# Kernel optimization log

Measured on AMD Instinct MI355X. Metric: run time of the kernel, lower is better.

Reference implementation:

```python
import jax, jax.numpy as jnp
import numpy as np

EMBED_DIM = 1024
FFN_DIM = 4096
N_QUBITS = 10


def setup_inputs() -> dict:
    key = jax.random.key(0)
    k_x, k_phi, k_w1, k_w2 = jax.random.split(key, 4)
    x = jax.random.normal(k_x, (8, 2048, EMBED_DIM), dtype=jnp.float32)
    # trainable RY angles, one per wire (torchquantum init ~ U(0, 2pi); any init works for a reference)
    ry_params = jax.random.uniform(k_phi, (N_QUBITS,), dtype=jnp.float32, minval=0.0, maxval=2.0 * np.pi)
    # nn.Linear(n_qubits, ffn_dim, bias=False): weight [ffn_dim, n_qubits]
    w1 = jax.random.normal(k_w1, (FFN_DIM, N_QUBITS), dtype=jnp.float32) / np.sqrt(N_QUBITS)
    # nn.Linear(ffn_dim, embed_dim, bias=False): weight [embed_dim, ffn_dim]
    w2 = jax.random.normal(k_w2, (EMBED_DIM, FFN_DIM), dtype=jnp.float32) / np.sqrt(FFN_DIM)
    return {"x": x, "ry_params": ry_params, "w1": w1, "w2": w2}


def reference(x, ry_params, w1, w2):
    # Quantum layer in closed form: wires are unentangled.
    # |0> --RX(x_i)--RY(phi_i)--> <Z_i> = cos(x_i) * cos(phi_i)
    # Only the first N_QUBITS features of each token are encoded.
    q_out = jnp.cos(x[..., :N_QUBITS]) * jnp.cos(ry_params)  # [B, S, nq]
    # dropout is identity in eval mode
    h = jnp.einsum('bsq,fq->bsf', q_out, w1)  # [B, S, ffn]
    h = jax.nn.relu(h)
    return jnp.einsum('bsf,ef->bse', h, w2)  # [B, S, embed]
```

## Files before the change

### kernel.cpp

```cpp
#include <hip/hip_runtime.h>
#include <stdint.h>

#define M_TOK   16384
#define EMBED   1024
#define FFN     4096
#define NQ      10

#define GK 4096
#define GN 1024
#define BK 64
#define NT (GK / BK)

typedef __attribute__((ext_vector_type(8))) short  bf16x8;
typedef __attribute__((ext_vector_type(4))) float  f32x4;
typedef __attribute__((ext_vector_type(8))) unsigned short u16x8;

static __device__ __forceinline__ unsigned short f2bf(float f) {
    union { float f; unsigned u; } v; v.f = f;
    unsigned r = v.u + 0x7FFF + ((v.u >> 16) & 1);
    return (unsigned short)(r >> 16);
}

__global__ __launch_bounds__(256) void compute_h(
    const float* __restrict__ x, const float* __restrict__ ry,
    const float* __restrict__ w1, unsigned short* __restrict__ h)
{
    __shared__ float cq[32 * 16];
    __shared__ float cry[NQ];

    const int tid = threadIdx.x;
    const int t0  = blockIdx.x * 32;
    const int fb  = blockIdx.y * 2048 + tid * 8;

    if (tid < NQ) cry[tid] = cosf(ry[tid]);
    for (int idx = tid; idx < 32 * NQ; idx += 256) {
        int t = idx / NQ;
        int i = idx - t * NQ;
        cq[t * 16 + i] = cosf(x[(size_t)(t0 + t) * EMBED + i]);
    }
    __syncthreads();

    float wf[8][NQ];
#pragma unroll
    for (int fi = 0; fi < 8; ++fi)
#pragma unroll
        for (int i = 0; i < NQ; ++i)
            wf[fi][i] = w1[(fb + fi) * NQ + i] * cry[i];

    for (int t = 0; t < 32; ++t) {
        const float4 c0 = *(const float4*)&cq[t * 16 + 0];
        const float4 c1 = *(const float4*)&cq[t * 16 + 4];
        const float2 c2 = *(const float2*)&cq[t * 16 + 8];
        u16x8 v;
#pragma unroll
        for (int fi = 0; fi < 8; ++fi) {
            float s = c0.x * wf[fi][0] + c0.y * wf[fi][1] + c0.z * wf[fi][2]
                    + c0.w * wf[fi][3] + c1.x * wf[fi][4] + c1.y * wf[fi][5]
                    + c1.z * wf[fi][6] + c1.w * wf[fi][7] + c2.x * wf[fi][8]
                    + c2.y * wf[fi][9];
            v[fi] = f2bf(fmaxf(s, 0.f));
        }
        *(u16x8*)(h + (size_t)(t0 + t) * FFN + fb) = v;
    }
}

__global__ __launch_bounds__(256) void conv_w2(
    const float* __restrict__ w2, unsigned short* __restrict__ o)
{
    const int idx = (blockIdx.x * 256 + threadIdx.x) * 8;
    float4 a = *(const float4*)(w2 + idx);
    float4 b = *(const float4*)(w2 + idx + 4);
    u16x8 v;
    v[0] = f2bf(a.x); v[1] = f2bf(a.y); v[2] = f2bf(a.z); v[3] = f2bf(a.w);
    v[4] = f2bf(b.x); v[5] = f2bf(b.y); v[6] = f2bf(b.z); v[7] = f2bf(b.w);
    *(u16x8*)(o + idx) = v;
}

#define GL2LDS(g, l) \
    __builtin_amdgcn_global_load_lds( \
        (const __attribute__((address_space(1))) void*)(g), \
        (__attribute__((address_space(3))) void*)(l), 16, 0, 0)

__global__ __launch_bounds__(512, 2) void gemm_bt(
    const unsigned short* __restrict__ A,
    const unsigned short* __restrict__ B,
    float* __restrict__ C)
{
    __shared__ __align__(16) unsigned short As[2][256 * BK];
    __shared__ __align__(16) unsigned short Bs[2][256 * BK];

    const int tid  = threadIdx.x;
    const int wv   = tid >> 6;
    const int lane = tid & 63;
    const int wm   = wv >> 2;
    const int wn   = wv & 3;

    const int bid = blockIdx.x;
    const int wg  = (bid & 7) * 32 + (bid >> 3);
    const int m0  = (wg >> 2) * 256;
    const int n0  = (wg & 3) * 256;

    const int srow8 = lane >> 3;
    const int schk  = (lane & 7) ^ srow8;
    const char* ag = (const char*)A +
        ((size_t)(m0 + wv * 16 + srow8) * GK + schk * 8) * 2;
    const char* bg = (const char*)B +
        ((size_t)(n0 + wv * 16 + srow8) * GK + schk * 8) * 2;
    const size_t ROW8 = (size_t)8 * GK * 2;
    const size_t HALF = (size_t)128 * GK * 2;

#define STAGE_A(buf, half, ko) do { \
    GL2LDS(ag + (ko) + (half) * HALF,        (char*)As[buf] + ((half) * 128 + wv * 16) * 128); \
    GL2LDS(ag + (ko) + (half) * HALF + ROW8, (char*)As[buf] + ((half) * 128 + wv * 16 + 8) * 128); \
} while (0)
#define STAGE_B(buf, half, ko) do { \
    GL2LDS(bg + (ko) + (half) * HALF,        (char*)Bs[buf] + ((half) * 128 + wv * 16) * 128); \
    GL2LDS(bg + (ko) + (half) * HALF + ROW8, (char*)Bs[buf] + ((half) * 128 + wv * 16 + 8) * 128); \
} while (0)

    const int rr  = lane & 15;
    const int fsw = lane & 7;
    const int cc  = lane >> 4;
#define CHOFF(s) ((((s) * 4 + cc) ^ fsw) * 16)
#define AFRAG(mh, i, s) (*(const bf16x8*)(At + (wm * 128 + (mh) * 64 + (i) * 16 + rr) * 128 + CHOFF(s)))
#define BFRAG(nh, j, s) (*(const bf16x8*)(Bt + (wn * 64 + (nh) * 32 + (j) * 16 + rr) * 128 + CHOFF(s)))

    f32x4 acc[8][4] = {};

    STAGE_A(0, 0, 0); STAGE_A(0, 1, 0);
    STAGE_B(0, 0, 0); STAGE_B(0, 1, 0);
    asm volatile("s_waitcnt vmcnt(0)" ::: "memory");
    __builtin_amdgcn_s_barrier();

#pragma unroll 1
    for (int T = 0; T < NT; ++T) {
        const char* At = (const char*)As[T & 1];
        const char* Bt = (const char*)Bs[T & 1];
        const int nb   = (T + 1) & 1;
        const size_t ko = (size_t)(T + 1) * 128;
        const bool st  = (T + 1 < NT);

        bf16x8 afr[2][4];
        bf16x8 b0r[2][2];
        bf16x8 b1r[2][2];

#pragma unroll
        for (int s = 0; s < 2; ++s) {
#pragma unroll
            for (int i = 0; i < 4; ++i) afr[s][i] = AFRAG(0, i, s);
#pragma unroll
            for (int j = 0; j < 2; ++j) b0r[s][j] = BFRAG(0, j, s);
        }
        if (st) { STAGE_A(nb, 0, ko); STAGE_A(nb, 1, ko); }
        __builtin_amdgcn_s_barrier();
        asm volatile("s_waitcnt lgkmcnt(0)" ::: "memory");
        __builtin_amdgcn_sched_barrier(0);
        __builtin_amdgcn_s_setprio(1);
#pragma unroll
        for (int s = 0; s < 2; ++s)
#pragma unroll
            for (int i = 0; i < 4; ++i)
#pragma unroll
                for (int j = 0; j < 2; ++j)
                    acc[i][j] = __builtin_amdgcn_mfma_f32_16x16x32_bf16(
                        afr[s][i], b0r[s][j], acc[i][j], 0, 0, 0);
        __builtin_amdgcn_s_setprio(0);
        __builtin_amdgcn_s_barrier();

#pragma unroll
        for (int s = 0; s < 2; ++s)
#pragma unroll
            for (int j = 0; j < 2; ++j) b1r[s][j] = BFRAG(1, j, s);
        if (st) { STAGE_B(nb, 0, ko); STAGE_B(nb, 1, ko); }
        __builtin_amdgcn_s_barrier();
        asm volatile("s_waitcnt lgkmcnt(0)" ::: "memory");
        __builtin_amdgcn_sched_barrier(0);
        __builtin_amdgcn_s_setprio(1);
#pragma unroll
        for (int s = 0; s < 2; ++s)
#pragma unroll
            for (int i = 0; i < 4; ++i)
#pragma unroll
                for (int j = 0; j < 2; ++j)
                    acc[i][2 + j] = __builtin_amdgcn_mfma_f32_16x16x32_bf16(
                        afr[s][i], b1r[s][j], acc[i][2 + j], 0, 0, 0);
        __builtin_amdgcn_s_setprio(0);
        __builtin_amdgcn_s_barrier();

#pragma unroll
        for (int s = 0; s < 2; ++s)
#pragma unroll
            for (int i = 0; i < 4; ++i) afr[s][i] = AFRAG(1, i, s);
        __builtin_amdgcn_s_barrier();
        asm volatile("s_waitcnt lgkmcnt(0)" ::: "memory");
        __builtin_amdgcn_sched_barrier(0);
        __builtin_amdgcn_s_setprio(1);
#pragma unroll
        for (int s = 0; s < 2; ++s)
#pragma unroll
            for (int i = 0; i < 4; ++i)
#pragma unroll
                for (int j = 0; j < 2; ++j)
                    acc[4 + i][2 + j] = __builtin_amdgcn_mfma_f32_16x16x32_bf16(
                        afr[s][i], b1r[s][j], acc[4 + i][2 + j], 0, 0, 0);
        __builtin_amdgcn_s_setprio(0);
        __builtin_amdgcn_s_barrier();

        __builtin_amdgcn_s_setprio(1);
#pragma unroll
        for (int s = 0; s < 2; ++s)
#pragma unroll
            for (int i = 0; i < 4; ++i)
#pragma unroll
                for (int j = 0; j < 2; ++j)
                    acc[4 + i][j] = __builtin_amdgcn_mfma_f32_16x16x32_bf16(
                        afr[s][i], b0r[s][j], acc[4 + i][j], 0, 0, 0);
        __builtin_amdgcn_s_setprio(0);
        asm volatile("s_waitcnt vmcnt(0)" ::: "memory");
        __builtin_amdgcn_s_barrier();
    }

    const int cn = lane & 15;
    const int rb = (lane >> 4) * 4;
#pragma unroll
    for (int i = 0; i < 8; ++i)
#pragma unroll
        for (int j = 0; j < 4; ++j)
#pragma unroll
            for (int r = 0; r < 4; ++r) {
                const int m = m0 + wm * 128 + i * 16 + rb + r;
                const int n = n0 + wn * 64 + j * 16 + cn;
                C[(size_t)m * GN + n] = acc[i][j][r];
            }
}

extern "C" void kernel_launch(void* const* d_in, const int* in_sizes, int n_in,
                              void* d_out, int out_size, void* d_ws, size_t ws_size,
                              hipStream_t stream) {
    const float* x  = (const float*)d_in[0];
    const float* ry = (const float*)d_in[1];
    const float* w1 = (const float*)d_in[2];
    const float* w2 = (const float*)d_in[3];
    float* out = (float*)d_out;

    unsigned short* h   = (unsigned short*)d_ws;
    unsigned short* w2b = (unsigned short*)((char*)d_ws +
                           (size_t)M_TOK * FFN * sizeof(unsigned short));

    compute_h<<<dim3(512, 2), 256, 0, stream>>>(x, ry, w1, h);
    conv_w2<<<dim3((EMBED * FFN) / (256 * 8)), 256, 0, stream>>>(w2, w2b);
    gemm_bt<<<dim3(256), 512, 0, stream>>>(h, w2b, out);
}
```

Before: 266.3 us.

## Unroll GEMM K-loop by two and prefetch B two tiles ahead

Restructures the main bf16 MFMA loop into a two-iteration unrolled body with a fixed LDS buffer per half. B tiles are now prefetched two k-steps ahead, and the global-to-LDS staging is spread across the four MFMA phases. The full vmcnt(0) wait at the end of each iteration becomes vmcnt(4), so loads stay in flight across iterations. This is meant to hide more global-load latency and remove the per-iteration drain. The cost is a more fragile wait-count schedule and redundant loads at the tail, which read offset 0.

```diff
diff --git a/kernel.cpp b/kernel.cpp
--- a/kernel.cpp
+++ b/kernel.cpp
@@ -122,103 +122,128 @@
     const int fsw = lane & 7;
     const int cc  = lane >> 4;
 #define CHOFF(s) ((((s) * 4 + cc) ^ fsw) * 16)
-#define AFRAG(mh, i, s) (*(const bf16x8*)(At + (wm * 128 + (mh) * 64 + (i) * 16 + rr) * 128 + CHOFF(s)))
-#define BFRAG(nh, j, s) (*(const bf16x8*)(Bt + (wn * 64 + (nh) * 32 + (j) * 16 + rr) * 128 + CHOFF(s)))
+#define AFRAGP(P, mh, i, s) (*(const bf16x8*)((P) + (wm * 128 + (mh) * 64 + (i) * 16 + rr) * 128 + CHOFF(s)))
+#define BFRAGP(P, nh, j, s) (*(const bf16x8*)((P) + (wn * 64 + (nh) * 32 + (j) * 16 + rr) * 128 + CHOFF(s)))
+
+#define LEADSYNC do { \
+    __builtin_amdgcn_s_barrier(); \
+    asm volatile("s_waitcnt lgkmcnt(0)" ::: "memory"); \
+    __builtin_amdgcn_sched_barrier(0); \
+} while (0)
 
     f32x4 acc[8][4] = {};
 
+#define MFMA16(I0, J0, AF, BF) do { \
+    __builtin_amdgcn_s_setprio(1); \
+    _Pragma("unroll") \
+    for (int s_ = 0; s_ < 2; ++s_) \
+        _Pragma("unroll") \
+        for (int i_ = 0; i_ < 4; ++i_) \
+            _Pragma("unroll") \
+            for (int j_ = 0; j_ < 2; ++j_) \
+                acc[(I0) + i_][(J0) + j_] = __builtin_amdgcn_mfma_f32_16x16x32_bf16( \
+                    AF[s_][i_], BF[s_][j_], acc[(I0) + i_][(J0) + j_], 0, 0, 0); \
+    __builtin_amdgcn_s_setprio(0); \
+} while (0)
+
+    STAGE_B(0, 0, 0); STAGE_B(0, 1, 0);
     STAGE_A(0, 0, 0); STAGE_A(0, 1, 0);
-    STAGE_B(0, 0, 0); STAGE_B(0, 1, 0);
+    STAGE_B(1, 0, 128); STAGE_B(1, 1, 128);
+    asm volatile("s_waitcnt vmcnt(4)" ::: "memory");
+    __builtin_amdgcn_s_barrier();
+
+#pragma unroll 1
+    for (int t = 0; t < NT / 2; ++t) {
+        const size_t kov = (size_t)(2 * t + 1) * 128;
+        const size_t ko2 = (2 * t + 2 < NT) ? (size_t)(2 * t + 2) * 128 : 0;
+        const size_t ko3 = (2 * t + 3 < NT) ? (size_t)(2 * t + 3) * 128 : 0;
+
+        bf16x8 afr[2][4], b0r[2][2], b1r[2][2];
+
+        {
+            const char* At = (const char*)As[0];
+            const char* Bt = (const char*)Bs[0];
+
+#pragma unroll
+            for (int s = 0; s < 2; ++s) {
+#pragma unroll
+                for (int j = 0; j < 2; ++j) b0r[s][j] = BFRAGP(Bt, 0, j, s);
+#pragma unroll
+                for (int i = 0; i < 4; ++i) afr[s][i] = AFRAGP(At, 0, i, s);
+            }
+            STAGE_A(1, 0, kov);
+            LEADSYNC;
+            MFMA16(0, 0, afr, b0r);
+            __builtin_amdgcn_s_barrier();
+
+#pragma unroll
+            for (int s = 0; s < 2; ++s)
+#pragma unroll
+                for (int j = 0; j < 2; ++j) b1r[s][j] = BFRAGP(Bt, 1, j, s);
+            STAGE_A(1, 1, kov);
+            LEADSYNC;
+            MFMA16(0, 2, afr, b1r);
+            __builtin_amdgcn_s_barrier();
+
+#pragma unroll
+            for (int s = 0; s < 2; ++s)
+#pragma unroll
+                for (int i = 0; i < 4; ++i) afr[s][i] = AFRAGP(At, 1, i, s);
+            STAGE_B(0, 0, ko2);
+            LEADSYNC;
+            MFMA16(4, 2, afr, b1r);
+            __builtin_amdgcn_s_barrier();
+
+            STAGE_B(0, 1, ko2);
+            LEADSYNC;
+            MFMA16(4, 0, afr, b0r);
+            asm volatile("s_waitcnt vmcnt(4)" ::: "memory");
+            __builtin_amdgcn_s_barrier();
+        }
+
+        {
+            const char* At = (const char*)As[1];
+            const char* Bt = (const char*)Bs[1];
+
+#pragma unroll
+            for (int s = 0; s < 2; ++s) {
+#pragma unroll
+                for (int j = 0; j < 2; ++j) b0r[s][j] = BFRAGP(Bt, 0, j, s);
+#pragma unroll
+                for (int i = 0; i < 4; ++i) afr[s][i] = AFRAGP(At, 0, i, s);
+            }
+            STAGE_A(0, 0, ko2);
+            LEADSYNC;
+            MFMA16(0, 0, afr, b0r);
+            __builtin_amdgcn_s_barrier();
+
+#pragma unroll
+            for (int s = 0; s < 2; ++s)
+#pragma unroll
+                for (int j = 0; j < 2; ++j) b1r[s][j] = BFRAGP(Bt, 1, j, s);
+            STAGE_A(0, 1, ko2);
+            LEADSYNC;
+            MFMA16(0, 2, afr, b1r);
+            __builtin_amdgcn_s_barrier();
+
+#pragma unroll
+            for (int s = 0; s < 2; ++s)
+#pragma unroll
+                for (int i = 0; i < 4; ++i) afr[s][i] = AFRAGP(At, 1, i, s);
+            STAGE_B(1, 0, ko3);
+            LEADSYNC;
+            MFMA16(4, 2, afr, b1r);
+            __builtin_amdgcn_s_barrier();
+
+            STAGE_B(1, 1, ko3);
+            LEADSYNC;
+            MFMA16(4, 0, afr, b0r);
+            asm volatile("s_waitcnt vmcnt(4)" ::: "memory");
+            __builtin_amdgcn_s_barrier();
+        }
+    }
+
     asm volatile("s_waitcnt vmcnt(0)" ::: "memory");
-    __builtin_amdgcn_s_barrier();
-
-#pragma unroll 1
-    for (int T = 0; T < NT; ++T) {
-        const char* At = (const char*)As[T & 1];
-        const char* Bt = (const char*)Bs[T & 1];
-        const int nb   = (T + 1) & 1;
-        const size_t ko = (size_t)(T + 1) * 128;
-        const bool st  = (T + 1 < NT);
-
-        bf16x8 afr[2][4];
-        bf16x8 b0r[2][2];
-        bf16x8 b1r[2][2];
-
-#pragma unroll
-        for (int s = 0; s < 2; ++s) {
-#pragma unroll
-            for (int i = 0; i < 4; ++i) afr[s][i] = AFRAG(0, i, s);
-#pragma unroll
-            for (int j = 0; j < 2; ++j) b0r[s][j] = BFRAG(0, j, s);
-        }
-        if (st) { STAGE_A(nb, 0, ko); STAGE_A(nb, 1, ko); }
-        __builtin_amdgcn_s_barrier();
-        asm volatile("s_waitcnt lgkmcnt(0)" ::: "memory");
-        __builtin_amdgcn_sched_barrier(0);
-        __builtin_amdgcn_s_setprio(1);
-#pragma unroll
-        for (int s = 0; s < 2; ++s)
-#pragma unroll
-            for (int i = 0; i < 4; ++i)
-#pragma unroll
-                for (int j = 0; j < 2; ++j)
-                    acc[i][j] = __builtin_amdgcn_mfma_f32_16x16x32_bf16(
-                        afr[s][i], b0r[s][j], acc[i][j], 0, 0, 0);
-        __builtin_amdgcn_s_setprio(0);
-        __builtin_amdgcn_s_barrier();
-
-#pragma unroll
-        for (int s = 0; s < 2; ++s)
-#pragma unroll
-            for (int j = 0; j < 2; ++j) b1r[s][j] = BFRAG(1, j, s);
-        if (st) { STAGE_B(nb, 0, ko); STAGE_B(nb, 1, ko); }
-        __builtin_amdgcn_s_barrier();
-        asm volatile("s_waitcnt lgkmcnt(0)" ::: "memory");
-        __builtin_amdgcn_sched_barrier(0);
-        __builtin_amdgcn_s_setprio(1);
-#pragma unroll
-        for (int s = 0; s < 2; ++s)
-#pragma unroll
-            for (int i = 0; i < 4; ++i)
-#pragma unroll
-                for (int j = 0; j < 2; ++j)
-                    acc[i][2 + j] = __builtin_amdgcn_mfma_f32_16x16x32_bf16(
-                        afr[s][i], b1r[s][j], acc[i][2 + j], 0, 0, 0);
-        __builtin_amdgcn_s_setprio(0);
-        __builtin_amdgcn_s_barrier();
-
-#pragma unroll
-        for (int s = 0; s < 2; ++s)
-#pragma unroll
-            for (int i = 0; i < 4; ++i) afr[s][i] = AFRAG(1, i, s);
-        __builtin_amdgcn_s_barrier();
-        asm volatile("s_waitcnt lgkmcnt(0)" ::: "memory");
-        __builtin_amdgcn_sched_barrier(0);
-        __builtin_amdgcn_s_setprio(1);
-#pragma unroll
-        for (int s = 0; s < 2; ++s)
-#pragma unroll
-            for (int i = 0; i < 4; ++i)
-#pragma unroll
-                for (int j = 0; j < 2; ++j)
-                    acc[4 + i][2 + j] = __builtin_amdgcn_mfma_f32_16x16x32_bf16(
-                        afr[s][i], b1r[s][j], acc[4 + i][2 + j], 0, 0, 0);
-        __builtin_amdgcn_s_setprio(0);
-        __builtin_amdgcn_s_barrier();
-
-        __builtin_amdgcn_s_setprio(1);
-#pragma unroll
-        for (int s = 0; s < 2; ++s)
-#pragma unroll
-            for (int i = 0; i < 4; ++i)
-#pragma unroll
-                for (int j = 0; j < 2; ++j)
-                    acc[4 + i][j] = __builtin_amdgcn_mfma_f32_16x16x32_bf16(
-                        afr[s][i], b0r[s][j], acc[4 + i][j], 0, 0, 0);
-        __builtin_amdgcn_s_setprio(0);
-        asm volatile("s_waitcnt vmcnt(0)" ::: "memory");
-        __builtin_amdgcn_s_barrier();
-    }
 
     const int cn = lane & 15;
     const int rb = (lane >> 4) * 4;
```

Result: slower. 278.6 us (+4.6%).
